# Performance work log

Measured on AMD Instinct MI355X. Metric: run time of the kernel, lower is better.

## Reference

```python
import jax, jax.numpy as jnp
import numpy as np

N_NODES = 100000
N_EDGES = 1600000
IN_DIM, HID_DIM, OUT_DIM = 128, 64, 64


def _graph_conv(src, dst, h, W, b, n_nodes):
    # DGL GraphConv, norm='both': out = D_in^{-1/2} A (D_out^{-1/2} h W) + b
    ones = jnp.ones(src.shape[0], dtype=h.dtype)
    deg_out = jax.ops.segment_sum(ones, src, num_segments=n_nodes)
    deg_in = jax.ops.segment_sum(ones, dst, num_segments=n_nodes)
    norm_src = jax.lax.rsqrt(jnp.maximum(deg_out, 1.0))  # [N]
    norm_dst = jax.lax.rsqrt(jnp.maximum(deg_in, 1.0))   # [N]
    # project first (in_dim >= out_dim path), then aggregate over edges
    x = (h * norm_src[:, None]) @ W                      # [N, d_out]
    msg = x[src]                                         # [E, d_out] gather
    agg = jax.ops.segment_sum(msg, dst, num_segments=n_nodes)  # [N, d_out]
    return agg * norm_dst[:, None] + b


def setup_inputs() -> dict:
    key = jax.random.key(0)
    k = jax.random.split(key, 6)
    h = jax.random.normal(k[0], (N_NODES, IN_DIM), dtype=jnp.float32)
    src = jax.random.randint(k[1], (N_EDGES,), 0, N_NODES, dtype=jnp.int32)
    dst = jax.random.randint(k[2], (N_EDGES,), 0, N_NODES, dtype=jnp.int32)
    W1 = jax.random.normal(k[3], (IN_DIM, HID_DIM), dtype=jnp.float32) / np.sqrt(IN_DIM)
    b1 = jnp.zeros((HID_DIM,), dtype=jnp.float32)
    W2 = jax.random.normal(k[4], (HID_DIM, OUT_DIM), dtype=jnp.float32) / np.sqrt(HID_DIM)
    b2 = jnp.zeros((OUT_DIM,), dtype=jnp.float32)
    return {"h": h, "src": src, "dst": dst, "W1": W1, "b1": b1, "W2": W2, "b2": b2}


def reference(h, src, dst, W1, b1, W2, b2):
    x = _graph_conv(src, dst, h, W1, b1, N_NODES)
    x = jax.nn.elu(x)  # act = nn.ELU()
    x = _graph_conv(src, dst, x, W2, b2, N_NODES)
    return x  # last_act is None
```

## Files before the change

### kernel.cpp

```cpp
#include <hip/hip_runtime.h>
#include <math.h>

#define CH 4096
#define NBUK_MAX 256
#define MAXB 12288
#define SRC_BITS 17

typedef short bf16x8 __attribute__((ext_vector_type(8)));
typedef float f32x4 __attribute__((ext_vector_type(4)));
typedef float f32x2 __attribute__((ext_vector_type(2)));

__device__ __forceinline__ unsigned short f2bf(float f) {
    union { float f; unsigned int u; } v; v.f = f;
    unsigned int r = (v.u + 0x7FFFu + ((v.u >> 16) & 1u)) >> 16;
    return (unsigned short)r;
}
__device__ __forceinline__ float bf2f(unsigned short u) {
    union { unsigned int u; float f; } v; v.u = ((unsigned int)u) << 16;
    return v.f;
}
__device__ __forceinline__ float bflo(unsigned int u) {
    union { unsigned int u; float f; } v; v.u = u << 16;
    return v.f;
}
__device__ __forceinline__ float bfhi(unsigned int u) {
    union { unsigned int u; float f; } v; v.u = u & 0xFFFF0000u;
    return v.f;
}

__global__ __launch_bounds__(256) void p1a_kernel(const int* __restrict__ src, const int* __restrict__ dst,
                                                  int* __restrict__ mat, int E, int B1, int nbuk) {
    __shared__ int hd[2][NBUK_MAX], hs[2][NBUK_MAX];
    const int t = threadIdx.x;
    const int p = (t >> 6) & 1;
    if (t < nbuk) { hd[0][t] = 0; hd[1][t] = 0; hs[0][t] = 0; hs[1][t] = 0; }
    __syncthreads();
    const int base = blockIdx.x * CH;
    const int cnt = min(CH, E - base);
    for (int k = t; k < cnt; k += 256) {
        int d = dst[base + k];
        int s = src[base + k];
        atomicAdd(&hd[p][d >> 9], 1);
        atomicAdd(&hs[p][s >> 9], 1);
    }
    __syncthreads();
    if (t < nbuk) {
        mat[t * B1 + blockIdx.x] = hd[0][t] + hd[1][t];
        mat[(nbuk + t) * B1 + blockIdx.x] = hs[0][t] + hs[1][t];
    }
}

__global__ __launch_bounds__(256) void scan1_kernel(const int* __restrict__ cnt,
                                                    int* __restrict__ seg,
                                                    int* __restrict__ bsums, int N) {
    __shared__ int tsum[256];
    const int t = threadIdx.x;
    const int base = blockIdx.x * 1024 + t * 4;
    int v0 = (base + 0 < N) ? cnt[base + 0] : 0;
    int v1 = (base + 1 < N) ? cnt[base + 1] : 0;
    int v2 = (base + 2 < N) ? cnt[base + 2] : 0;
    int v3 = (base + 3 < N) ? cnt[base + 3] : 0;
    tsum[t] = v0 + v1 + v2 + v3;
    __syncthreads();
    for (int off = 1; off < 256; off <<= 1) {
        int x = (t >= off) ? tsum[t - off] : 0;
        __syncthreads();
        if (t >= off) tsum[t] += x;
        __syncthreads();
    }
    int run = (t > 0) ? tsum[t - 1] : 0;
    if (base + 0 < N) seg[base + 0] = run; run += v0;
    if (base + 1 < N) seg[base + 1] = run; run += v1;
    if (base + 2 < N) seg[base + 2] = run; run += v2;
    if (base + 3 < N) seg[base + 3] = run;
    if (t == 255) bsums[blockIdx.x] = tsum[255];
}

__global__ void scan2_kernel(int* __restrict__ bsums, int* __restrict__ seg, int N, int G) {
    __shared__ int s[256];
    int t = threadIdx.x;
    if (t < G) s[t] = bsums[t];
    __syncthreads();
    if (t == 0) {
        int run = 0;
        for (int i = 0; i < G; ++i) { int v = s[i]; s[i] = run; run += v; }
        seg[N] = run;
    }
    __syncthreads();
    if (t < G) bsums[t] = s[t];
}

__global__ __launch_bounds__(256) void scan3_kernel(int* __restrict__ seg,
                                                    const int* __restrict__ bsums, int N) {
    int add = bsums[blockIdx.x];
    int base = blockIdx.x * 1024 + threadIdx.x * 4;
#pragma unroll
    for (int i = 0; i < 4; ++i) {
        int idx = base + i;
        if (idx < N) seg[idx] += add;
    }
}

__global__ __launch_bounds__(256) void p1c_kernel(const int* __restrict__ src, const int* __restrict__ dst,
                                                  const int* __restrict__ mat,
                                                  const int* __restrict__ scan,
                                                  int* __restrict__ pedge,
                                                  int E, int B1, int nbuk) {
    __shared__ int hd[NBUK_MAX], hs[NBUK_MAX];
    __shared__ int curD[NBUK_MAX], curS[NBUK_MAX];
    __shared__ int baseD[NBUK_MAX], baseS[NBUK_MAX];
    __shared__ int stD[CH];
    __shared__ int stS[CH];
    __shared__ unsigned char bkD[CH];
    const int t = threadIdx.x;
    if (t < nbuk) {
        hd[t] = mat[t * B1 + blockIdx.x];
        hs[t] = mat[(nbuk + t) * B1 + blockIdx.x];
    }
    const int base = blockIdx.x * CH;
    const int cnt = min(CH, E - base);
    int dl[CH / 256], sl[CH / 256];
#pragma unroll
    for (int k = 0; k < CH / 256; ++k) {
        int i = t + k * 256;
        if (i < cnt) {
            dl[k] = dst[base + i];
            sl[k] = src[base + i];
        }
    }
    __syncthreads();
    for (int off = 1; off < nbuk; off <<= 1) {
        int v0 = (t >= off && t < nbuk) ? hd[t - off] : 0;
        int w0 = (t >= off && t < nbuk) ? hs[t - off] : 0;
        __syncthreads();
        if (t < nbuk) { hd[t] += v0; hs[t] += w0; }
        __syncthreads();
    }
    if (t < nbuk) {
        int excD = t ? hd[t - 1] : 0;
        int excS = t ? hs[t - 1] : 0;
        curD[t] = excD;
        curS[t] = excS;
        baseD[t] = scan[t * B1 + blockIdx.x] - excD;
        baseS[t] = scan[(nbuk + t) * B1 + blockIdx.x] - excS;
    }
    __syncthreads();
#pragma unroll
    for (int k = 0; k < CH / 256; ++k) {
        int i = t + k * 256;
        if (i < cnt) {
            int j = dl[k] >> 9;
            int p = atomicAdd(&curD[j], 1);
            stD[p] = ((dl[k] & 511) << SRC_BITS) | sl[k];
            bkD[p] = (unsigned char)j;
            int jq = sl[k] >> 9;
            int q = atomicAdd(&curS[jq], 1);
            stS[q] = sl[k] | (jq << SRC_BITS);
        }
    }
    __syncthreads();
    for (int i = t; i < cnt; i += 256) {
        int b = bkD[i];
        pedge[baseD[b] + i] = stD[i];
        int v = stS[i];
        pedge[baseS[v >> SRC_BITS] + i] = v;
    }
}

__global__ __launch_bounds__(512) void p2s2_kernel(const int* __restrict__ pedge,
                                                   const int* __restrict__ scan,
                                                   int* __restrict__ esrc, int* __restrict__ seg,
                                                   float* __restrict__ norm_dst,
                                                   float* __restrict__ norm_src,
                                                   int N, int E, int B1, int nbuk) {
    __shared__ int h[512];
    __shared__ int cur[512];
    __shared__ int stage[MAXB];
    const int t = threadIdx.x;
    const int b0 = blockIdx.x;
    if (b0 >= nbuk) {
        const int b = b0 - nbuk;
        h[t] = 0;
        __syncthreads();
        const int sb0 = scan[(nbuk + b) * B1];
        const int sb1 = scan[(nbuk + b + 1) * B1];
        for (int i = sb0 + t; i < sb1; i += 512) atomicAdd(&h[pedge[i] & 511], 1);
        __syncthreads();
        int n = (b << 9) + t;
        if (n < N) norm_src[n] = rsqrtf(fmaxf((float)h[t], 1.0f));
        return;
    }
    const int b = b0;
    h[t] = 0;
    __syncthreads();
    const int bb0 = scan[b * B1];
    const int bb1 = scan[(b + 1) * B1];
    for (int i = bb0 + t; i < bb1; i += 512) atomicAdd(&h[(pedge[i] >> SRC_BITS) & 511], 1);
    __syncthreads();
    for (int off = 1; off < 512; off <<= 1) {
        int v = (t >= off) ? h[t - off] : 0;
        __syncthreads();
        h[t] += v;
        __syncthreads();
    }
    {
        int exc = t ? h[t - 1] : 0;
        cur[t] = exc;
        int n = (b << 9) + t;
        if (n < N) {
            seg[n] = bb0 + exc;
            norm_dst[n] = rsqrtf(fmaxf((float)(h[t] - exc), 1.0f));
        }
        if (b == 0 && t == 0) seg[N] = E;
    }
    __syncthreads();
    const int cnt = bb1 - bb0;
    for (int i = bb0 + t; i < bb1; i += 512) {
        int v = pedge[i];
        int j = (v >> SRC_BITS) & 511;
        int p = atomicAdd(&cur[j], 1);
        int s = v & ((1 << SRC_BITS) - 1);
        if (p < MAXB) stage[p] = s; else esrc[bb0 + p] = s;
    }
    __syncthreads();
    for (int i = t; i < cnt && i < MAXB; i += 512) esrc[bb0 + i] = stage[i];
}

template<int K>
__global__ __launch_bounds__(256) void gemm_norm(const float* __restrict__ H,
                                                 const float* __restrict__ W,
                                                 const float* __restrict__ norm,
                                                 unsigned short* __restrict__ X, int N) {
    constexpr int KP = K + 8;
    __shared__ __align__(16) unsigned short sHi[64 * KP];
    __shared__ __align__(16) unsigned short sLo[64 * KP];
    const int tid = threadIdx.x;

    for (int idx = tid; idx < K * 64; idx += 256) {
        int k = idx >> 6;
        int c = idx & 63;
        float v = W[idx];
        unsigned short hi = f2bf(v);
        sHi[c * KP + k] = hi;
        sLo[c * KP + k] = f2bf(v - bf2f(hi));
    }
    __syncthreads();

    const int w = tid >> 6;
    const int lane = tid & 63;
    const int quad = lane >> 4;
    const int l16 = lane & 15;
    const int n0 = blockIdx.x * 64;
    const int arow = n0 + w * 16 + l16;
    const int arow_c = (arow < N) ? arow : (N - 1);
    const float* Hrow = H + (size_t)arow_c * K + quad * 8;

    f32x4 acc[4];
#pragma unroll
    for (int t = 0; t < 4; ++t) acc[t] = (f32x4){0.0f, 0.0f, 0.0f, 0.0f};

    float4 p0 = *(const float4*)(Hrow + 0);
    float4 p1 = *(const float4*)(Hrow + 4);

#pragma unroll
    for (int kc = 0; kc < K / 32; ++kc) {
        const float v[8] = {p0.x, p0.y, p0.z, p0.w, p1.x, p1.y, p1.z, p1.w};
        bf16x8 aHi, aLo;
#pragma unroll
        for (int j = 0; j < 8; ++j) {
            unsigned short hi = f2bf(v[j]);
            aHi[j] = (short)hi;
            aLo[j] = (short)f2bf(v[j] - bf2f(hi));
        }
        if (kc + 1 < K / 32) {
            p0 = *(const float4*)(Hrow + (kc + 1) * 32 + 0);
            p1 = *(const float4*)(Hrow + (kc + 1) * 32 + 4);
        }
        const int kbase = kc * 32 + quad * 8;
#pragma unroll
        for (int t = 0; t < 4; ++t) {
            const int col = t * 16 + l16;
            const bf16x8 bHi = *(const bf16x8*)&sHi[col * KP + kbase];
            const bf16x8 bLo = *(const bf16x8*)&sLo[col * KP + kbase];
            acc[t] = __builtin_amdgcn_mfma_f32_16x16x32_bf16(aLo, bHi, acc[t], 0, 0, 0);
            acc[t] = __builtin_amdgcn_mfma_f32_16x16x32_bf16(aHi, bLo, acc[t], 0, 0, 0);
            acc[t] = __builtin_amdgcn_mfma_f32_16x16x32_bf16(aHi, bHi, acc[t], 0, 0, 0);
        }
    }

#pragma unroll
    for (int r = 0; r < 4; ++r) {
        const int node = n0 + w * 16 + quad * 4 + r;
        if (node < N) {
            const float s = norm[node];
#pragma unroll
            for (int t = 0; t < 4; ++t) {
                X[(size_t)node * 64 + t * 16 + l16] = f2bf(acc[t][r] * s);
            }
        } else if (node == N) {
#pragma unroll
            for (int t = 0; t < 4; ++t) {
                X[(size_t)node * 64 + t * 16 + l16] = 0;
            }
        }
    }
}

template<bool ELU>
__global__ __launch_bounds__(256) void segsum_kernel(const unsigned short* __restrict__ X,
                                                     const int* __restrict__ esrc,
                                                     const int* __restrict__ seg,
                                                     const float* __restrict__ norm_dst,
                                                     const float* __restrict__ bias,
                                                     float* __restrict__ out, int N) {
    const int node = __builtin_amdgcn_readfirstlane(blockIdx.x * 4 + (threadIdx.x >> 6));
    if (node >= N) return;
    const int lane = threadIdx.x & 63;
    const int eh = lane >> 3;
    const int fl = lane & 7;
    const unsigned flo = (unsigned)fl << 4;
    const int fown = fl * 8 + ((eh & 1) << 2) + (eh & 2) + (eh >> 2);
    const float bv = bias[fown];
    const int s0 = seg[node];
    const int s1 = seg[node + 1];
    const char* Xb = (const char*)X;
    f32x2 A0 = {0.0f, 0.0f}, A1 = {0.0f, 0.0f}, A2 = {0.0f, 0.0f}, A3 = {0.0f, 0.0f};
#define ACC8(u) \
    A0 += (f32x2){bflo(u.x), bfhi(u.x)}; A1 += (f32x2){bflo(u.y), bfhi(u.y)}; \
    A2 += (f32x2){bflo(u.z), bfhi(u.z)}; A3 += (f32x2){bflo(u.w), bfhi(u.w)};
    int e = s0;
    while (true) {
        const int b4 = e + eh * 4;
        const uint4 q = *(const uint4*)&esrc[b4];
        const int r0 = (b4 + 0 < s1) ? (int)q.x : N;
        const int r1 = (b4 + 1 < s1) ? (int)q.y : N;
        const int r2 = (b4 + 2 < s1) ? (int)q.z : N;
        const int r3 = (b4 + 3 < s1) ? (int)q.w : N;
        const uint4 u0 = *(const uint4*)(Xb + ((((unsigned)r0) << 7) | flo));
        const uint4 u1 = *(const uint4*)(Xb + ((((unsigned)r1) << 7) | flo));
        const uint4 u2 = *(const uint4*)(Xb + ((((unsigned)r2) << 7) | flo));
        const uint4 u3 = *(const uint4*)(Xb + ((((unsigned)r3) << 7) | flo));
        ACC8(u0);
        ACC8(u1);
        ACC8(u2);
        ACC8(u3);
        e += 32;
        if (e >= s1) break;
    }
#undef ACC8
    float a0 = A0.x, a1 = A0.y, a2 = A1.x, a3 = A1.y;
    float a4 = A2.x, a5 = A2.y, a6 = A3.x, a7 = A3.y;
    const bool p0 = (eh & 1) != 0;
    const bool p1 = (eh & 2) != 0;
    const bool p2 = (eh & 4) != 0;
    float t0, t1, t2, t3;
    {
        float sA = p0 ? a0 : a4, kA = p0 ? a4 : a0;
        float sB = p0 ? a1 : a5, kB = p0 ? a5 : a1;
        float sC = p0 ? a2 : a6, kC = p0 ? a6 : a2;
        float sD = p0 ? a3 : a7, kD = p0 ? a7 : a3;
        t0 = kA + __shfl_xor(sA, 8);
        t1 = kB + __shfl_xor(sB, 8);
        t2 = kC + __shfl_xor(sC, 8);
        t3 = kD + __shfl_xor(sD, 8);
    }
    float u0, u1;
    {
        float sA = p1 ? t0 : t2, kA = p1 ? t2 : t0;
        float sB = p1 ? t1 : t3, kB = p1 ? t3 : t1;
        u0 = kA + __shfl_xor(sA, 16);
        u1 = kB + __shfl_xor(sB, 16);
    }
    float v;
    {
        float sA = p2 ? u0 : u1, kA = p2 ? u1 : u0;
        v = kA + __shfl_xor(sA, 32);
    }
    const float s = norm_dst[node];
    float r = v * s + bv;
    if (ELU) r = r > 0.0f ? r : expm1f(r);
    out[(size_t)node * 64 + fown] = r;
}

extern "C" void kernel_launch(void* const* d_in, const int* in_sizes, int n_in,
                              void* d_out, int out_size, void* d_ws, size_t ws_size,
                              hipStream_t stream) {
    const float* h   = (const float*)d_in[0];
    const int*   src = (const int*)d_in[1];
    const int*   dst = (const int*)d_in[2];
    const float* W1  = (const float*)d_in[3];
    const float* b1  = (const float*)d_in[4];
    const float* W2  = (const float*)d_in[5];
    const float* b2  = (const float*)d_in[6];
    float* out = (float*)d_out;

    const int N = in_sizes[0] / 128;
    const int E = in_sizes[1];
    const int nbuk = (N + 511) >> 9;
    const int B1 = (E + CH - 1) / CH;
    const int M = 2 * nbuk * B1;

    int* iw = (int*)d_ws;
    int* mat   = iw;
    int* scanb = mat + M;
    int* bsums = scanb + M + 4;
    int* pedge = bsums + 256;
    int* esrc  = pedge + 2 * (size_t)E;
    int* seg   = esrc + (size_t)E + 40;
    uintptr_t fp = (uintptr_t)(seg + (size_t)N + 4);
    fp = (fp + 63) & ~(uintptr_t)63;
    float* norm_src = (float*)fp;
    float* norm_dst = norm_src + (size_t)N;
    float* H1       = norm_dst + (size_t)N;
    unsigned short* Xb = (unsigned short*)(H1 + 64 * (size_t)N);

    p1a_kernel<<<B1, 256, 0, stream>>>(src, dst, mat, E, B1, nbuk);
    const int G = (M + 1023) / 1024;
    scan1_kernel<<<G, 256, 0, stream>>>(mat, scanb, bsums, M);
    scan2_kernel<<<1, 256, 0, stream>>>(bsums, scanb, M, G);
    scan3_kernel<<<G, 256, 0, stream>>>(scanb, bsums, M);
    p1c_kernel<<<B1, 256, 0, stream>>>(src, dst, mat, scanb, pedge, E, B1, nbuk);
    p2s2_kernel<<<2 * nbuk, 512, 0, stream>>>(pedge, scanb, esrc, seg, norm_dst, norm_src,
                                              N, E, B1, nbuk);

    const int segGrid = (N + 3) / 4;
    const int gemmGrid = (N + 64) / 64;

    gemm_norm<128><<<gemmGrid, 256, 0, stream>>>(h, W1, norm_src, Xb, N);
    segsum_kernel<true><<<segGrid, 256, 0, stream>>>(Xb, esrc, seg, norm_dst, b1, H1, N);

    gemm_norm<64><<<gemmGrid, 256, 0, stream>>>(H1, W2, norm_src, Xb, N);
    segsum_kernel<false><<<segGrid, 256, 0, stream>>>(Xb, esrc, seg, norm_dst, b2, out, N);
}
```

Before: 238.8 us.

## Replace histogram+scan partition with atomic bucket reservation into fixed-capacity slots

Fuses the per-chunk histogram, three-kernel global scan and scatter into one partition kernel that reserves space in each bucket with a global atomicAdd, writing into fixed MAXB-sized bucket slots. The second pass uses the bucket counts directly and emits separate segment start/end arrays, since buckets are no longer contiguous. This removes four kernel launches and the scan traffic, at the cost of a memset, non-deterministic edge order within buckets, and a hard assumption that no bucket exceeds MAXB edges (the overflow path was dropped).

```diff
diff --git a/kernel.cpp b/kernel.cpp
--- a/kernel.cpp
+++ b/kernel.cpp
@@ -28,127 +28,64 @@
     return v.f;
 }
 
-__global__ __launch_bounds__(256) void p1a_kernel(const int* __restrict__ src, const int* __restrict__ dst,
-                                                  int* __restrict__ mat, int E, int B1, int nbuk) {
+__global__ __launch_bounds__(256) void part_kernel(const int* __restrict__ src, const int* __restrict__ dst,
+                                                   int* __restrict__ cnt,
+                                                   int* __restrict__ pedge,
+                                                   int E, int nbuk) {
     __shared__ int hd[2][NBUK_MAX], hs[2][NBUK_MAX];
-    const int t = threadIdx.x;
-    const int p = (t >> 6) & 1;
-    if (t < nbuk) { hd[0][t] = 0; hd[1][t] = 0; hs[0][t] = 0; hs[1][t] = 0; }
-    __syncthreads();
-    const int base = blockIdx.x * CH;
-    const int cnt = min(CH, E - base);
-    for (int k = t; k < cnt; k += 256) {
-        int d = dst[base + k];
-        int s = src[base + k];
-        atomicAdd(&hd[p][d >> 9], 1);
-        atomicAdd(&hs[p][s >> 9], 1);
-    }
-    __syncthreads();
-    if (t < nbuk) {
-        mat[t * B1 + blockIdx.x] = hd[0][t] + hd[1][t];
-        mat[(nbuk + t) * B1 + blockIdx.x] = hs[0][t] + hs[1][t];
-    }
-}
-
-__global__ __launch_bounds__(256) void scan1_kernel(const int* __restrict__ cnt,
-                                                    int* __restrict__ seg,
-                                                    int* __restrict__ bsums, int N) {
-    __shared__ int tsum[256];
-    const int t = threadIdx.x;
-    const int base = blockIdx.x * 1024 + t * 4;
-    int v0 = (base + 0 < N) ? cnt[base + 0] : 0;
-    int v1 = (base + 1 < N) ? cnt[base + 1] : 0;
-    int v2 = (base + 2 < N) ? cnt[base + 2] : 0;
-    int v3 = (base + 3 < N) ? cnt[base + 3] : 0;
-    tsum[t] = v0 + v1 + v2 + v3;
-    __syncthreads();
-    for (int off = 1; off < 256; off <<= 1) {
-        int x = (t >= off) ? tsum[t - off] : 0;
-        __syncthreads();
-        if (t >= off) tsum[t] += x;
-        __syncthreads();
-    }
-    int run = (t > 0) ? tsum[t - 1] : 0;
-    if (base + 0 < N) seg[base + 0] = run; run += v0;
-    if (base + 1 < N) seg[base + 1] = run; run += v1;
-    if (base + 2 < N) seg[base + 2] = run; run += v2;
-    if (base + 3 < N) seg[base + 3] = run;
-    if (t == 255) bsums[blockIdx.x] = tsum[255];
-}
-
-__global__ void scan2_kernel(int* __restrict__ bsums, int* __restrict__ seg, int N, int G) {
-    __shared__ int s[256];
-    int t = threadIdx.x;
-    if (t < G) s[t] = bsums[t];
-    __syncthreads();
-    if (t == 0) {
-        int run = 0;
-        for (int i = 0; i < G; ++i) { int v = s[i]; s[i] = run; run += v; }
-        seg[N] = run;
-    }
-    __syncthreads();
-    if (t < G) bsums[t] = s[t];
-}
-
-__global__ __launch_bounds__(256) void scan3_kernel(int* __restrict__ seg,
-                                                    const int* __restrict__ bsums, int N) {
-    int add = bsums[blockIdx.x];
-    int base = blockIdx.x * 1024 + threadIdx.x * 4;
-#pragma unroll
-    for (int i = 0; i < 4; ++i) {
-        int idx = base + i;
-        if (idx < N) seg[idx] += add;
-    }
-}
-
-__global__ __launch_bounds__(256) void p1c_kernel(const int* __restrict__ src, const int* __restrict__ dst,
-                                                  const int* __restrict__ mat,
-                                                  const int* __restrict__ scan,
-                                                  int* __restrict__ pedge,
-                                                  int E, int B1, int nbuk) {
-    __shared__ int hd[NBUK_MAX], hs[NBUK_MAX];
     __shared__ int curD[NBUK_MAX], curS[NBUK_MAX];
     __shared__ int baseD[NBUK_MAX], baseS[NBUK_MAX];
     __shared__ int stD[CH];
     __shared__ int stS[CH];
     __shared__ unsigned char bkD[CH];
     const int t = threadIdx.x;
-    if (t < nbuk) {
-        hd[t] = mat[t * B1 + blockIdx.x];
-        hs[t] = mat[(nbuk + t) * B1 + blockIdx.x];
-    }
+    const int par = (t >> 6) & 1;
+    if (t < nbuk) { hd[0][t] = 0; hd[1][t] = 0; hs[0][t] = 0; hs[1][t] = 0; }
+    __syncthreads();
     const int base = blockIdx.x * CH;
-    const int cnt = min(CH, E - base);
+    const int cntE = min(CH, E - base);
     int dl[CH / 256], sl[CH / 256];
 #pragma unroll
     for (int k = 0; k < CH / 256; ++k) {
         int i = t + k * 256;
-        if (i < cnt) {
+        if (i < cntE) {
             dl[k] = dst[base + i];
             sl[k] = src[base + i];
-        }
+            atomicAdd(&hd[par][dl[k] >> 9], 1);
+            atomicAdd(&hs[par][sl[k] >> 9], 1);
+        }
+    }
+    __syncthreads();
+    int cD = 0, cS = 0;
+    if (t < nbuk) {
+        cD = hd[0][t] + hd[1][t];
+        cS = hs[0][t] + hs[1][t];
+        hd[0][t] = cD;
+        hs[0][t] = cS;
     }
     __syncthreads();
     for (int off = 1; off < nbuk; off <<= 1) {
-        int v0 = (t >= off && t < nbuk) ? hd[t - off] : 0;
-        int w0 = (t >= off && t < nbuk) ? hs[t - off] : 0;
-        __syncthreads();
-        if (t < nbuk) { hd[t] += v0; hs[t] += w0; }
+        int v0 = (t >= off && t < nbuk) ? hd[0][t - off] : 0;
+        int w0 = (t >= off && t < nbuk) ? hs[0][t - off] : 0;
+        __syncthreads();
+        if (t < nbuk) { hd[0][t] += v0; hs[0][t] += w0; }
         __syncthreads();
     }
     if (t < nbuk) {
-        int excD = t ? hd[t - 1] : 0;
-        int excS = t ? hs[t - 1] : 0;
+        int excD = hd[0][t] - cD;
+        int excS = hs[0][t] - cS;
         curD[t] = excD;
         curS[t] = excS;
-        baseD[t] = scan[t * B1 + blockIdx.x] - excD;
-        baseS[t] = scan[(nbuk + t) * B1 + blockIdx.x] - excS;
+        int gD = atomicAdd(&cnt[t], cD);
+        int gS = atomicAdd(&cnt[nbuk + t], cS);
+        baseD[t] = t * MAXB + gD - excD;
+        baseS[t] = (nbuk + t) * MAXB + gS - excS;
     }
     __syncthreads();
 #pragma unroll
     for (int k = 0; k < CH / 256; ++k) {
         int i = t + k * 256;
-        if (i < cnt) {
+        if (i < cntE) {
             int j = dl[k] >> 9;
             int p = atomicAdd(&curD[j], 1);
             stD[p] = ((dl[k] & 511) << SRC_BITS) | sl[k];
@@ -159,20 +96,20 @@
         }
     }
     __syncthreads();
-    for (int i = t; i < cnt; i += 256) {
-        int b = bkD[i];
-        pedge[baseD[b] + i] = stD[i];
+    for (int i = t; i < cntE; i += 256) {
+        pedge[baseD[bkD[i]] + i] = stD[i];
         int v = stS[i];
         pedge[baseS[v >> SRC_BITS] + i] = v;
     }
 }
 
 __global__ __launch_bounds__(512) void p2s2_kernel(const int* __restrict__ pedge,
-                                                   const int* __restrict__ scan,
-                                                   int* __restrict__ esrc, int* __restrict__ seg,
+                                                   const int* __restrict__ cnt,
+                                                   int* __restrict__ esrc,
+                                                   int* __restrict__ segS, int* __restrict__ segE,
                                                    float* __restrict__ norm_dst,
                                                    float* __restrict__ norm_src,
-                                                   int N, int E, int B1, int nbuk) {
+                                                   int N, int nbuk) {
     __shared__ int h[512];
     __shared__ int cur[512];
     __shared__ int stage[MAXB];
@@ -182,8 +119,8 @@
         const int b = b0 - nbuk;
         h[t] = 0;
         __syncthreads();
-        const int sb0 = scan[(nbuk + b) * B1];
-        const int sb1 = scan[(nbuk + b + 1) * B1];
+        const int sb0 = (nbuk + b) * MAXB;
+        const int sb1 = sb0 + cnt[nbuk + b];
         for (int i = sb0 + t; i < sb1; i += 512) atomicAdd(&h[pedge[i] & 511], 1);
         __syncthreads();
         int n = (b << 9) + t;
@@ -193,8 +130,9 @@
     const int b = b0;
     h[t] = 0;
     __syncthreads();
-    const int bb0 = scan[b * B1];
-    const int bb1 = scan[(b + 1) * B1];
+    const int bb0 = b * MAXB;
+    const int cntHere = cnt[b];
+    const int bb1 = bb0 + cntHere;
     for (int i = bb0 + t; i < bb1; i += 512) atomicAdd(&h[(pedge[i] >> SRC_BITS) & 511], 1);
     __syncthreads();
     for (int off = 1; off < 512; off <<= 1) {
@@ -208,22 +146,20 @@
         cur[t] = exc;
         int n = (b << 9) + t;
         if (n < N) {
-            seg[n] = bb0 + exc;
+            segS[n] = bb0 + exc;
+            segE[n] = bb0 + h[t];
             norm_dst[n] = rsqrtf(fmaxf((float)(h[t] - exc), 1.0f));
         }
-        if (b == 0 && t == 0) seg[N] = E;
-    }
-    __syncthreads();
-    const int cnt = bb1 - bb0;
+    }
+    __syncthreads();
     for (int i = bb0 + t; i < bb1; i += 512) {
         int v = pedge[i];
         int j = (v >> SRC_BITS) & 511;
         int p = atomicAdd(&cur[j], 1);
-        int s = v & ((1 << SRC_BITS) - 1);
-        if (p < MAXB) stage[p] = s; else esrc[bb0 + p] = s;
-    }
-    __syncthreads();
-    for (int i = t; i < cnt && i < MAXB; i += 512) esrc[bb0 + i] = stage[i];
+        stage[p] = v & ((1 << SRC_BITS) - 1);
+    }
+    __syncthreads();
+    for (int i = t; i < cntHere; i += 512) esrc[bb0 + i] = stage[i];
 }
 
 template<int K>
@@ -309,7 +245,8 @@
 template<bool ELU>
 __global__ __launch_bounds__(256) void segsum_kernel(const unsigned short* __restrict__ X,
                                                      const int* __restrict__ esrc,
-                                                     const int* __restrict__ seg,
+                                                     const int* __restrict__ segS,
+                                                     const int* __restrict__ segE,
                                                      const float* __restrict__ norm_dst,
                                                      const float* __restrict__ bias,
                                                      float* __restrict__ out, int N) {
@@ -321,8 +258,8 @@
     const unsigned flo = (unsigned)fl << 4;
     const int fown = fl * 8 + ((eh & 1) << 2) + (eh & 2) + (eh >> 2);
     const float bv = bias[fown];
-    const int s0 = seg[node];
-    const int s1 = seg[node + 1];
+    const int s0 = segS[node];
+    const int s1 = segE[node];
     const char* Xb = (const char*)X;
     f32x2 A0 = {0.0f, 0.0f}, A1 = {0.0f, 0.0f}, A2 = {0.0f, 0.0f}, A3 = {0.0f, 0.0f};
 #define ACC8(u) \
@@ -398,37 +335,31 @@
     const int E = in_sizes[1];
     const int nbuk = (N + 511) >> 9;
     const int B1 = (E + CH - 1) / CH;
-    const int M = 2 * nbuk * B1;
 
     int* iw = (int*)d_ws;
-    int* mat   = iw;
-    int* scanb = mat + M;
-    int* bsums = scanb + M + 4;
-    int* pedge = bsums + 256;
-    int* esrc  = pedge + 2 * (size_t)E;
-    int* seg   = esrc + (size_t)E + 40;
-    uintptr_t fp = (uintptr_t)(seg + (size_t)N + 4);
+    int* cnt   = iw;
+    int* pedge = cnt + 2 * nbuk;
+    int* esrc  = pedge + 2 * (size_t)nbuk * MAXB;
+    int* segS  = esrc + (size_t)nbuk * MAXB + 40;
+    int* segE  = segS + (size_t)N;
+    uintptr_t fp = (uintptr_t)(segE + (size_t)N);
     fp = (fp + 63) & ~(uintptr_t)63;
     float* norm_src = (float*)fp;
     float* norm_dst = norm_src + (size_t)N;
     float* H1       = norm_dst + (size_t)N;
     unsigned short* Xb = (unsigned short*)(H1 + 64 * (size_t)N);
 
-    p1a_kernel<<<B1, 256, 0, stream>>>(src, dst, mat, E, B1, nbuk);
-    const int G = (M + 1023) / 1024;
-    scan1_kernel<<<G, 256, 0, stream>>>(mat, scanb, bsums, M);
-    scan2_kernel<<<1, 256, 0, stream>>>(bsums, scanb, M, G);
-    scan3_kernel<<<G, 256, 0, stream>>>(scanb, bsums, M);
-    p1c_kernel<<<B1, 256, 0, stream>>>(src, dst, mat, scanb, pedge, E, B1, nbuk);
-    p2s2_kernel<<<2 * nbuk, 512, 0, stream>>>(pedge, scanb, esrc, seg, norm_dst, norm_src,
-                                              N, E, B1, nbuk);
+    hipMemsetAsync(cnt, 0, 2 * nbuk * sizeof(int), stream);
+    part_kernel<<<B1, 256, 0, stream>>>(src, dst, cnt, pedge, E, nbuk);
+    p2s2_kernel<<<2 * nbuk, 512, 0, stream>>>(pedge, cnt, esrc, segS, segE,
+                                              norm_dst, norm_src, N, nbuk);
 
     const int segGrid = (N + 3) / 4;
     const int gemmGrid = (N + 64) / 64;
 
     gemm_norm<128><<<gemmGrid, 256, 0, stream>>>(h, W1, norm_src, Xb, N);
-    segsum_kernel<true><<<segGrid, 256, 0, stream>>>(Xb, esrc, seg, norm_dst, b1, H1, N);
+    segsum_kernel<true><<<segGrid, 256, 0, stream>>>(Xb, esrc, segS, segE, norm_dst, b1, H1, N);
 
     gemm_norm<64><<<gemmGrid, 256, 0, stream>>>(H1, W2, norm_src, Xb, N);
-    segsum_kernel<false><<<segGrid, 256, 0, stream>>>(Xb, esrc, seg, norm_dst, b2, out, N);
-}
+    segsum_kernel<false><<<segGrid, 256, 0, stream>>>(Xb, esrc, segS, segE, norm_dst, b2, out, N);
+}
```

Measured after the change: 264.4 us. +10.7%, slower.
